# Optimization experiments

Measured on AMD Instinct MI355X. Metric: run time of the kernel, lower is better.

The kernel has to match this reference:

```python
import jax, jax.numpy as jnp
import numpy as np

C = 1.0
TEMPERATURE = 1.0
EPS = 1e-10
N, D = 8192, 512


def setup_inputs() -> dict:
    key = jax.random.key(0)
    k1, k2 = jax.random.split(key)
    # scale so embeddings lie inside the unit (Poincare) ball: norms ~0.5
    scale = 0.5 / np.sqrt(D)
    audio = jax.random.normal(k1, (N, D), dtype=jnp.float32) * scale
    text = jax.random.normal(k2, (N, D), dtype=jnp.float32) * scale
    labels = jnp.arange(N, dtype=jnp.int32)
    return {"audio_features": audio, "text_features": text, "labels": labels}


def _hyperbolic_similarity(a, b):
    # pairwise squared distance via norm expansion (avoids N x N x D tensor)
    a2 = jnp.sum(a * a, axis=-1)            # [N]
    b2 = jnp.sum(b * b, axis=-1)            # [M]
    diff_sq = a2[:, None] + b2[None, :] - 2.0 * (a @ b.T)  # [N, M]
    a2c = jnp.minimum(a2, 1.0 - EPS)
    b2c = jnp.minimum(b2, 1.0 - EPS)
    denom = jnp.maximum((1.0 - a2c)[:, None] * (1.0 - b2c)[None, :], EPS)
    arg = jnp.maximum(1.0 + 2.0 * diff_sq / denom, 1.0 + EPS)
    dist = jnp.arccosh(arg) / jnp.sqrt(jnp.asarray(C, a.dtype))
    return -dist / TEMPERATURE


def _cross_entropy(logits, labels):
    logp = jax.nn.log_softmax(logits, axis=-1)
    picked = jnp.take_along_axis(logp, labels[:, None], axis=-1)[:, 0]
    return -jnp.mean(picked)


def reference(audio_features, text_features, labels):
    sim = _hyperbolic_similarity(audio_features, text_features)  # [N, M]
    loss_audio = _cross_entropy(sim, labels)
    loss_text = _cross_entropy(sim.T, labels)
    return (loss_audio + loss_text) * 0.5
```

## Files before the change

### kernel.cpp

```cpp
#include <hip/hip_runtime.h>
#include <hip/hip_bf16.h>


#define NROWS 8192
#define DDIM  512
#define BM 128
#define BN 128
#define BK 64
#define NT (DDIM / BK)

typedef __attribute__((ext_vector_type(8))) short bf16x8;
typedef __attribute__((ext_vector_type(4))) float f32x4;

constexpr float EPSF = 1e-10f;

#define GLOAD_LDS16(g, l)                                                        \
    __builtin_amdgcn_global_load_lds(                                            \
        (const __attribute__((address_space(1))) void*)(g),                      \
        (__attribute__((address_space(3))) void*)(l), 16, 0, 0)

__device__ inline unsigned short f2bf(float f) {
    union { float f; unsigned int u; } x; x.f = f;
    unsigned int r = x.u + 0x7fffu + ((x.u >> 16) & 1u);
    return (unsigned short)(r >> 16);
}

__global__ __launch_bounds__(256) void convert_norms(const float* __restrict__ audio,
                                                     const float* __restrict__ text,
                                                     unsigned short* __restrict__ Ab,
                                                     unsigned short* __restrict__ Bb,
                                                     float* __restrict__ a2,
                                                     float* __restrict__ b2,
                                                     float* __restrict__ diag) {
    int wave = threadIdx.x >> 6;
    int lane = threadIdx.x & 63;
    int row  = blockIdx.x * 4 + wave;
    const float* ra = audio + (size_t)row * DDIM + lane * 8;
    const float* rt = text  + (size_t)row * DDIM + lane * 8;
    float4 a0 = *(const float4*)(ra), a1 = *(const float4*)(ra + 4);
    float4 t0 = *(const float4*)(rt), t1 = *(const float4*)(rt + 4);

    float sa = a0.x*a0.x + a0.y*a0.y + a0.z*a0.z + a0.w*a0.w
             + a1.x*a1.x + a1.y*a1.y + a1.z*a1.z + a1.w*a1.w;
    float st = t0.x*t0.x + t0.y*t0.y + t0.z*t0.z + t0.w*t0.w
             + t1.x*t1.x + t1.y*t1.y + t1.z*t1.z + t1.w*t1.w;
    float dt = a0.x*t0.x + a0.y*t0.y + a0.z*t0.z + a0.w*t0.w
             + a1.x*t1.x + a1.y*t1.y + a1.z*t1.z + a1.w*t1.w;

    unsigned short ua[8], ut[8];
    ua[0]=f2bf(a0.x); ua[1]=f2bf(a0.y); ua[2]=f2bf(a0.z); ua[3]=f2bf(a0.w);
    ua[4]=f2bf(a1.x); ua[5]=f2bf(a1.y); ua[6]=f2bf(a1.z); ua[7]=f2bf(a1.w);
    ut[0]=f2bf(t0.x); ut[1]=f2bf(t0.y); ut[2]=f2bf(t0.z); ut[3]=f2bf(t0.w);
    ut[4]=f2bf(t1.x); ut[5]=f2bf(t1.y); ut[6]=f2bf(t1.z); ut[7]=f2bf(t1.w);
    *(uint4*)(Ab + (size_t)row * DDIM + lane * 8) = *(const uint4*)ua;
    *(uint4*)(Bb + (size_t)row * DDIM + lane * 8) = *(const uint4*)ut;

    #pragma unroll
    for (int m = 1; m < 64; m <<= 1) {
        sa += __shfl_xor(sa, m);
        st += __shfl_xor(st, m);
        dt += __shfl_xor(dt, m);
    }
    if (lane == 0) {
        a2[row] = sa;
        b2[row] = st;
        float a2c  = fminf(sa, 1.0f - EPSF);
        float b2c  = fminf(st, 1.0f - EPSF);
        float diff = sa + st - 2.0f * dt;
        float den  = fmaxf((1.0f - a2c) * (1.0f - b2c), EPSF);
        float arg  = fmaxf(1.0f + 2.0f * diff / den, 1.0f + EPSF);
        diag[row]  = -logf(arg + sqrtf(arg * arg - 1.0f));
    }
}

__global__ __launch_bounds__(256) void hyper_gemm(
    const unsigned short* __restrict__ A, const unsigned short* __restrict__ B,
    const float* __restrict__ a2, const float* __restrict__ b2,
    float* __restrict__ rowsum, float* __restrict__ colsum) {

    __shared__ char lds[2 * 32768];

    const int tid  = threadIdx.x;
    const int lane = tid & 63;
    const int w    = tid >> 6;
    const int wr   = w >> 1, wc = w & 1;

    const int bid = blockIdx.x;
    const int idx = bid >> 3;
    const int by  = (bid & 7) * 8 + (idx & 7);
    const int bx  = idx >> 3;
    const int i0 = by * BM;
    const int j0 = bx * BN;

    const int g  = lane >> 4;
    const int cl = lane & 15;

    const int srow = lane >> 3;
    const int scol = ((lane & 7) ^ srow) * 8;
    const char* aP[4]; const char* bP[4]; int ldsOff[4];
    #pragma unroll
    for (int c = 0; c < 4; ++c) {
        int row = w * 32 + c * 8 + srow;
        aP[c] = (const char*)(A + (size_t)(i0 + row) * DDIM + scol);
        bP[c] = (const char*)(B + (size_t)(j0 + row) * DDIM + scol);
        ldsOff[c] = w * 4096 + c * 1024;
    }

    int offA[4][2], offB[4][2];
    #pragma unroll
    for (int mi = 0; mi < 4; ++mi) {
        int rowA = wr * 64 + mi * 16 + cl;
        int rowB = wc * 64 + mi * 16 + cl;
        #pragma unroll
        for (int kh = 0; kh < 2; ++kh) {
            int cb = (kh * 32 + g * 8) * 2;
            offA[mi][kh] = rowA * 128 + (cb ^ ((rowA & 7) << 4));
            offB[mi][kh] = 16384 + rowB * 128 + (cb ^ ((rowB & 7) << 4));
        }
    }

    f32x4 acc[4][4];
    #pragma unroll
    for (int mi = 0; mi < 4; ++mi)
        #pragma unroll
        for (int ni = 0; ni < 4; ++ni)
            acc[mi][ni] = (f32x4)0.0f;

#define STAGE(buf, t)                                                     \
    do {                                                                  \
        _Pragma("unroll")                                                 \
        for (int c = 0; c < 4; ++c) {                                     \
            GLOAD_LDS16(aP[c] + (t) * (BK * 2),                           \
                        lds + (buf) * 32768 + ldsOff[c]);                 \
            GLOAD_LDS16(bP[c] + (t) * (BK * 2),                           \
                        lds + (buf) * 32768 + 16384 + ldsOff[c]);         \
        }                                                                 \
    } while (0)

#define COMPUTE(buf)                                                      \
    do {                                                                  \
        _Pragma("unroll")                                                 \
        for (int kh = 0; kh < 2; ++kh) {                                  \
            bf16x8 af[4], bfr[4];                                         \
            _Pragma("unroll")                                             \
            for (int mi = 0; mi < 4; ++mi)                                \
                af[mi] = *(const bf16x8*)(lds + (buf) * 32768 + offA[mi][kh]); \
            _Pragma("unroll")                                             \
            for (int ni = 0; ni < 4; ++ni)                                \
                bfr[ni] = *(const bf16x8*)(lds + (buf) * 32768 + offB[ni][kh]); \
            _Pragma("unroll")                                             \
            for (int mi = 0; mi < 4; ++mi)                                \
                _Pragma("unroll")                                         \
                for (int ni = 0; ni < 4; ++ni)                            \
                    acc[mi][ni] = __builtin_amdgcn_mfma_f32_16x16x32_bf16(\
                        af[mi], bfr[ni], acc[mi][ni], 0, 0, 0);           \
        }                                                                 \
    } while (0)

    STAGE(0, 0);
    __syncthreads();
    #pragma unroll
    for (int t = 0; t < NT; ++t) {
        if (t + 1 < NT) STAGE((t + 1) & 1, t + 1);
        COMPUTE(t & 1);
        if (t + 1 < NT) __syncthreads();
    }
#undef STAGE
#undef COMPUTE

    float B2c[4], fb[4];
    #pragma unroll
    for (int ni = 0; ni < 4; ++ni) {
        float B2 = b2[j0 + wc * 64 + ni * 16 + cl];
        B2c[ni] = B2;
        fb[ni] = __builtin_amdgcn_rcpf(1.0f - fminf(B2, 1.0f - EPSF));
    }

    float cp[4] = {0.f, 0.f, 0.f, 0.f};
    #pragma unroll
    for (int mi = 0; mi < 4; ++mi) {
        #pragma unroll
        for (int reg = 0; reg < 4; ++reg) {
            int   gi  = i0 + wr * 64 + mi * 16 + g * 4 + reg;
            float A2  = a2[gi];
            float fa  = 2.0f * __builtin_amdgcn_rcpf(1.0f - fminf(A2, 1.0f - EPSF));
            float rsum = 0.f;
            #pragma unroll
            for (int ni = 0; ni < 4; ++ni) {
                float dot  = acc[mi][ni][reg];
                float diff = fmaf(-2.0f, dot, A2 + B2c[ni]);
                float arg  = fmaf(diff * fa, fb[ni], 1.0f);
                arg = fmaxf(arg, 1.0f);
                float sq = sqrtf(fmaf(arg, arg, -1.0f));
                float e  = arg - sq;
                rsum += e;
                cp[ni] += e;
            }
            float v = rsum;
            v += __shfl_xor(v, 1); v += __shfl_xor(v, 2);
            v += __shfl_xor(v, 4); v += __shfl_xor(v, 8);
            if (cl == 0) atomicAdd(&rowsum[gi], v);
        }
    }
    #pragma unroll
    for (int ni = 0; ni < 4; ++ni) {
        float v = cp[ni];
        v += __shfl_xor(v, 16); v += __shfl_xor(v, 32);
        if (g == 0) atomicAdd(&colsum[j0 + wc * 64 + ni * 16 + cl], v);
    }
}

__global__ __launch_bounds__(256) void finalize(const float* __restrict__ rowsum,
                                                const float* __restrict__ colsum,
                                                const float* __restrict__ diag,
                                                float* __restrict__ out) {
    int i = blockIdx.x * 256 + threadIdx.x;
    float s = logf(rowsum[i]) + logf(colsum[i]) - 2.0f * diag[i];
    #pragma unroll
    for (int m = 1; m < 64; m <<= 1) s += __shfl_xor(s, m);
    if ((threadIdx.x & 63) == 0)
        atomicAdd(out, s * (1.0f / (2.0f * NROWS)));
}

extern "C" void kernel_launch(void* const* d_in, const int* in_sizes, int n_in,
                              void* d_out, int out_size, void* d_ws, size_t ws_size,
                              hipStream_t stream) {
    const float* audio = (const float*)d_in[0];
    const float* text  = (const float*)d_in[1];
    float* out = (float*)d_out;

    char* ws = (char*)d_ws;
    const size_t BF = (size_t)NROWS * DDIM * sizeof(unsigned short);
    unsigned short* Abf = (unsigned short*)ws;
    unsigned short* Bbf = (unsigned short*)(ws + BF);
    float* a2     = (float*)(ws + 2 * BF);
    float* b2     = a2 + NROWS;
    float* rowsum = b2 + NROWS;
    float* colsum = rowsum + NROWS;
    float* diag   = colsum + NROWS;

    hipMemsetAsync(rowsum, 0, 2 * NROWS * sizeof(float), stream);
    hipMemsetAsync(out, 0, sizeof(float), stream);
    convert_norms<<<NROWS / 4, 256, 0, stream>>>(audio, text, Abf, Bbf, a2, b2, diag);
    hyper_gemm<<<(NROWS / BM) * (NROWS / BN), 256, 0, stream>>>(Abf, Bbf, a2, b2, rowsum, colsum);
    finalize<<<NROWS / 256, 256, 0, stream>>>(rowsum, colsum, diag, out);
}
```

Measured before the change: 227.0 us.

## Enlarge GEMM tile to 256x256 with 8 waves per block

Doubles the block tile to 256x256 with 512 threads (8 waves in a 2x4 layout), each wave computing a 128x64 sub-tile. LDS staging per buffer doubles to 64 KB, and the block-index swizzle is reworked for the 32x32 grid. The goal is more data reuse per LDS byte and fewer atomic partial-sum writes. In exchange, accumulator register use doubles, the 128 KB of LDS allows only one block per CU, and the grid shrinks to 1024 blocks, which may hurt latency hiding.

```diff
diff --git a/kernel.cpp b/kernel.cpp
--- a/kernel.cpp
+++ b/kernel.cpp
@@ -4,10 +4,11 @@
 
 #define NROWS 8192
 #define DDIM  512
-#define BM 128
-#define BN 128
+#define BM 256
+#define BN 256
 #define BK 64
 #define NT (DDIM / BK)
+#define LDSBUF 65536
 
 typedef __attribute__((ext_vector_type(8))) short bf16x8;
 typedef __attribute__((ext_vector_type(4))) float f32x4;
@@ -73,22 +74,23 @@
     }
 }
 
-__global__ __launch_bounds__(256) void hyper_gemm(
+__global__ __launch_bounds__(512) void hyper_gemm(
     const unsigned short* __restrict__ A, const unsigned short* __restrict__ B,
     const float* __restrict__ a2, const float* __restrict__ b2,
     float* __restrict__ rowsum, float* __restrict__ colsum) {
 
-    __shared__ char lds[2 * 32768];
+    __shared__ char lds[2 * LDSBUF];
 
     const int tid  = threadIdx.x;
     const int lane = tid & 63;
     const int w    = tid >> 6;
-    const int wr   = w >> 1, wc = w & 1;
+    const int wm   = w >> 2;
+    const int wn   = w & 3;
 
     const int bid = blockIdx.x;
-    const int idx = bid >> 3;
-    const int by  = (bid & 7) * 8 + (idx & 7);
-    const int bx  = idx >> 3;
+    const int swz = (bid & 7) * 128 + (bid >> 3);
+    const int by  = swz >> 5;
+    const int bx  = swz & 31;
     const int i0 = by * BM;
     const int j0 = bx * BN;
 
@@ -106,22 +108,29 @@
         ldsOff[c] = w * 4096 + c * 1024;
     }
 
-    int offA[4][2], offB[4][2];
-    #pragma unroll
-    for (int mi = 0; mi < 4; ++mi) {
-        int rowA = wr * 64 + mi * 16 + cl;
-        int rowB = wc * 64 + mi * 16 + cl;
+    int offA[8][2], offB[4][2];
+    #pragma unroll
+    for (int mi = 0; mi < 8; ++mi) {
+        int rowA = wm * 128 + mi * 16 + cl;
         #pragma unroll
         for (int kh = 0; kh < 2; ++kh) {
             int cb = (kh * 32 + g * 8) * 2;
             offA[mi][kh] = rowA * 128 + (cb ^ ((rowA & 7) << 4));
-            offB[mi][kh] = 16384 + rowB * 128 + (cb ^ ((rowB & 7) << 4));
         }
     }
-
-    f32x4 acc[4][4];
-    #pragma unroll
-    for (int mi = 0; mi < 4; ++mi)
+    #pragma unroll
+    for (int ni = 0; ni < 4; ++ni) {
+        int rowB = wn * 64 + ni * 16 + cl;
+        #pragma unroll
+        for (int kh = 0; kh < 2; ++kh) {
+            int cb = (kh * 32 + g * 8) * 2;
+            offB[ni][kh] = 32768 + rowB * 128 + (cb ^ ((rowB & 7) << 4));
+        }
+    }
+
+    f32x4 acc[8][4];
+    #pragma unroll
+    for (int mi = 0; mi < 8; ++mi)
         #pragma unroll
         for (int ni = 0; ni < 4; ++ni)
             acc[mi][ni] = (f32x4)0.0f;
@@ -131,9 +140,9 @@
         _Pragma("unroll")                                                 \
         for (int c = 0; c < 4; ++c) {                                     \
             GLOAD_LDS16(aP[c] + (t) * (BK * 2),                           \
-                        lds + (buf) * 32768 + ldsOff[c]);                 \
+                        lds + (buf) * LDSBUF + ldsOff[c]);                \
             GLOAD_LDS16(bP[c] + (t) * (BK * 2),                           \
-                        lds + (buf) * 32768 + 16384 + ldsOff[c]);         \
+                        lds + (buf) * LDSBUF + 32768 + ldsOff[c]);        \
         }                                                                 \
     } while (0)
 
@@ -141,19 +150,19 @@
     do {                                                                  \
         _Pragma("unroll")                                                 \
         for (int kh = 0; kh < 2; ++kh) {                                  \
-            bf16x8 af[4], bfr[4];                                         \
+            bf16x8 af[8], bv[4];                                          \
             _Pragma("unroll")                                             \
-            for (int mi = 0; mi < 4; ++mi)                                \
-                af[mi] = *(const bf16x8*)(lds + (buf) * 32768 + offA[mi][kh]); \
+            for (int mi = 0; mi < 8; ++mi)                                \
+                af[mi] = *(const bf16x8*)(lds + (buf) * LDSBUF + offA[mi][kh]); \
             _Pragma("unroll")                                             \
             for (int ni = 0; ni < 4; ++ni)                                \
-                bfr[ni] = *(const bf16x8*)(lds + (buf) * 32768 + offB[ni][kh]); \
+                bv[ni] = *(const bf16x8*)(lds + (buf) * LDSBUF + offB[ni][kh]); \
             _Pragma("unroll")                                             \
-            for (int mi = 0; mi < 4; ++mi)                                \
+            for (int mi = 0; mi < 8; ++mi)                                \
                 _Pragma("unroll")                                         \
                 for (int ni = 0; ni < 4; ++ni)                            \
                     acc[mi][ni] = __builtin_amdgcn_mfma_f32_16x16x32_bf16(\
-                        af[mi], bfr[ni], acc[mi][ni], 0, 0, 0);           \
+                        af[mi], bv[ni], acc[mi][ni], 0, 0, 0);            \
         }                                                                 \
     } while (0)
 
@@ -171,17 +180,17 @@
     float B2c[4], fb[4];
     #pragma unroll
     for (int ni = 0; ni < 4; ++ni) {
-        float B2 = b2[j0 + wc * 64 + ni * 16 + cl];
+        float B2 = b2[j0 + wn * 64 + ni * 16 + cl];
         B2c[ni] = B2;
         fb[ni] = __builtin_amdgcn_rcpf(1.0f - fminf(B2, 1.0f - EPSF));
     }
 
     float cp[4] = {0.f, 0.f, 0.f, 0.f};
     #pragma unroll
-    for (int mi = 0; mi < 4; ++mi) {
+    for (int mi = 0; mi < 8; ++mi) {
         #pragma unroll
         for (int reg = 0; reg < 4; ++reg) {
-            int   gi  = i0 + wr * 64 + mi * 16 + g * 4 + reg;
+            int   gi  = i0 + wm * 128 + mi * 16 + g * 4 + reg;
             float A2  = a2[gi];
             float fa  = 2.0f * __builtin_amdgcn_rcpf(1.0f - fminf(A2, 1.0f - EPSF));
             float rsum = 0.f;
@@ -206,7 +215,7 @@
     for (int ni = 0; ni < 4; ++ni) {
         float v = cp[ni];
         v += __shfl_xor(v, 16); v += __shfl_xor(v, 32);
-        if (g == 0) atomicAdd(&colsum[j0 + wc * 64 + ni * 16 + cl], v);
+        if (g == 0) atomicAdd(&colsum[j0 + wn * 64 + ni * 16 + cl], v);
     }
 }
 
@@ -242,6 +251,6 @@
     hipMemsetAsync(rowsum, 0, 2 * NROWS * sizeof(float), stream);
     hipMemsetAsync(out, 0, sizeof(float), stream);
     convert_norms<<<NROWS / 4, 256, 0, stream>>>(audio, text, Abf, Bbf, a2, b2, diag);
-    hyper_gemm<<<(NROWS / BM) * (NROWS / BN), 256, 0, stream>>>(Abf, Bbf, a2, b2, rowsum, colsum);
+    hyper_gemm<<<(NROWS / BM) * (NROWS / BN), 512, 0, stream>>>(Abf, Bbf, a2, b2, rowsum, colsum);
     finalize<<<NROWS / 256, 256, 0, stream>>>(rowsum, colsum, diag, out);
 }
```

Result: slower. 277.5 us (+22.2%).

## Use 8 waves per GEMM block and single-block finalize reduction

Applied to the files above, without the earlier changes.

The hyperbolic GEMM block grows from 4 to 8 waves. Each wave now computes a 64x32 sub-tile instead of 64x64, which halves the accumulator registers and global-to-LDS loads per wave and is meant to raise latency hiding and occupancy. The finalize step becomes a single 1024-thread block that reduces through shared memory and writes the output directly, removing the output memset and the atomics. The trade-off is more LDS reads per MFMA (the A fragments are re-read by more waves) and more row and column atomics in the epilogue.

```diff
diff --git a/kernel.cpp b/kernel.cpp
--- a/kernel.cpp
+++ b/kernel.cpp
@@ -8,6 +8,7 @@
 #define BN 128
 #define BK 64
 #define NT (DDIM / BK)
+#define LDSBUF 32768
 
 typedef __attribute__((ext_vector_type(8))) short bf16x8;
 typedef __attribute__((ext_vector_type(4))) float f32x4;
@@ -73,17 +74,18 @@
     }
 }
 
-__global__ __launch_bounds__(256) void hyper_gemm(
+__global__ __launch_bounds__(512, 4) void hyper_gemm(
     const unsigned short* __restrict__ A, const unsigned short* __restrict__ B,
     const float* __restrict__ a2, const float* __restrict__ b2,
     float* __restrict__ rowsum, float* __restrict__ colsum) {
 
-    __shared__ char lds[2 * 32768];
+    __shared__ char lds[2 * LDSBUF];
 
     const int tid  = threadIdx.x;
     const int lane = tid & 63;
     const int w    = tid >> 6;
-    const int wr   = w >> 1, wc = w & 1;
+    const int wm   = w >> 2;
+    const int wn   = w & 3;
 
     const int bid = blockIdx.x;
     const int idx = bid >> 3;
@@ -97,43 +99,50 @@
 
     const int srow = lane >> 3;
     const int scol = ((lane & 7) ^ srow) * 8;
-    const char* aP[4]; const char* bP[4]; int ldsOff[4];
-    #pragma unroll
-    for (int c = 0; c < 4; ++c) {
-        int row = w * 32 + c * 8 + srow;
+    const char* aP[2]; const char* bP[2]; int ldsOff[2];
+    #pragma unroll
+    for (int c = 0; c < 2; ++c) {
+        int row = w * 16 + c * 8 + srow;
         aP[c] = (const char*)(A + (size_t)(i0 + row) * DDIM + scol);
         bP[c] = (const char*)(B + (size_t)(j0 + row) * DDIM + scol);
-        ldsOff[c] = w * 4096 + c * 1024;
-    }
-
-    int offA[4][2], offB[4][2];
+        ldsOff[c] = w * 2048 + c * 1024;
+    }
+
+    int offA[4][2], offB[2][2];
     #pragma unroll
     for (int mi = 0; mi < 4; ++mi) {
-        int rowA = wr * 64 + mi * 16 + cl;
-        int rowB = wc * 64 + mi * 16 + cl;
+        int rowA = wm * 64 + mi * 16 + cl;
         #pragma unroll
         for (int kh = 0; kh < 2; ++kh) {
             int cb = (kh * 32 + g * 8) * 2;
             offA[mi][kh] = rowA * 128 + (cb ^ ((rowA & 7) << 4));
-            offB[mi][kh] = 16384 + rowB * 128 + (cb ^ ((rowB & 7) << 4));
         }
     }
-
-    f32x4 acc[4][4];
+    #pragma unroll
+    for (int ni = 0; ni < 2; ++ni) {
+        int rowB = wn * 32 + ni * 16 + cl;
+        #pragma unroll
+        for (int kh = 0; kh < 2; ++kh) {
+            int cb = (kh * 32 + g * 8) * 2;
+            offB[ni][kh] = 16384 + rowB * 128 + (cb ^ ((rowB & 7) << 4));
+        }
+    }
+
+    f32x4 acc[4][2];
     #pragma unroll
     for (int mi = 0; mi < 4; ++mi)
         #pragma unroll
-        for (int ni = 0; ni < 4; ++ni)
+        for (int ni = 0; ni < 2; ++ni)
             acc[mi][ni] = (f32x4)0.0f;
 
 #define STAGE(buf, t)                                                     \
     do {                                                                  \
         _Pragma("unroll")                                                 \
-        for (int c = 0; c < 4; ++c) {                                     \
+        for (int c = 0; c < 2; ++c) {                                     \
             GLOAD_LDS16(aP[c] + (t) * (BK * 2),                           \
-                        lds + (buf) * 32768 + ldsOff[c]);                 \
+                        lds + (buf) * LDSBUF + ldsOff[c]);                \
             GLOAD_LDS16(bP[c] + (t) * (BK * 2),                           \
-                        lds + (buf) * 32768 + 16384 + ldsOff[c]);         \
+                        lds + (buf) * LDSBUF + 16384 + ldsOff[c]);        \
         }                                                                 \
     } while (0)
 
@@ -141,19 +150,19 @@
     do {                                                                  \
         _Pragma("unroll")                                                 \
         for (int kh = 0; kh < 2; ++kh) {                                  \
-            bf16x8 af[4], bfr[4];                                         \
+            bf16x8 af[4], bv[2];                                          \
             _Pragma("unroll")                                             \
             for (int mi = 0; mi < 4; ++mi)                                \
-                af[mi] = *(const bf16x8*)(lds + (buf) * 32768 + offA[mi][kh]); \
+                af[mi] = *(const bf16x8*)(lds + (buf) * LDSBUF + offA[mi][kh]); \
             _Pragma("unroll")                                             \
-            for (int ni = 0; ni < 4; ++ni)                                \
-                bfr[ni] = *(const bf16x8*)(lds + (buf) * 32768 + offB[ni][kh]); \
+            for (int ni = 0; ni < 2; ++ni)                                \
+                bv[ni] = *(const bf16x8*)(lds + (buf) * LDSBUF + offB[ni][kh]); \
             _Pragma("unroll")                                             \
             for (int mi = 0; mi < 4; ++mi)                                \
                 _Pragma("unroll")                                         \
-                for (int ni = 0; ni < 4; ++ni)                            \
+                for (int ni = 0; ni < 2; ++ni)                            \
                     acc[mi][ni] = __builtin_amdgcn_mfma_f32_16x16x32_bf16(\
-                        af[mi], bfr[ni], acc[mi][ni], 0, 0, 0);           \
+                        af[mi], bv[ni], acc[mi][ni], 0, 0, 0);            \
         }                                                                 \
     } while (0)
 
@@ -168,25 +177,25 @@
 #undef STAGE
 #undef COMPUTE
 
-    float B2c[4], fb[4];
-    #pragma unroll
-    for (int ni = 0; ni < 4; ++ni) {
-        float B2 = b2[j0 + wc * 64 + ni * 16 + cl];
+    float B2c[2], fb[2];
+    #pragma unroll
+    for (int ni = 0; ni < 2; ++ni) {
+        float B2 = b2[j0 + wn * 32 + ni * 16 + cl];
         B2c[ni] = B2;
         fb[ni] = __builtin_amdgcn_rcpf(1.0f - fminf(B2, 1.0f - EPSF));
     }
 
-    float cp[4] = {0.f, 0.f, 0.f, 0.f};
+    float cp[2] = {0.f, 0.f};
     #pragma unroll
     for (int mi = 0; mi < 4; ++mi) {
         #pragma unroll
         for (int reg = 0; reg < 4; ++reg) {
-            int   gi  = i0 + wr * 64 + mi * 16 + g * 4 + reg;
+            int   gi  = i0 + wm * 64 + mi * 16 + g * 4 + reg;
             float A2  = a2[gi];
             float fa  = 2.0f * __builtin_amdgcn_rcpf(1.0f - fminf(A2, 1.0f - EPSF));
             float rsum = 0.f;
             #pragma unroll
-            for (int ni = 0; ni < 4; ++ni) {
+            for (int ni = 0; ni < 2; ++ni) {
                 float dot  = acc[mi][ni][reg];
                 float diff = fmaf(-2.0f, dot, A2 + B2c[ni]);
                 float arg  = fmaf(diff * fa, fb[ni], 1.0f);
@@ -203,23 +212,32 @@
         }
     }
     #pragma unroll
-    for (int ni = 0; ni < 4; ++ni) {
+    for (int ni = 0; ni < 2; ++ni) {
         float v = cp[ni];
         v += __shfl_xor(v, 16); v += __shfl_xor(v, 32);
-        if (g == 0) atomicAdd(&colsum[j0 + wc * 64 + ni * 16 + cl], v);
-    }
-}
-
-__global__ __launch_bounds__(256) void finalize(const float* __restrict__ rowsum,
-                                                const float* __restrict__ colsum,
-                                                const float* __restrict__ diag,
-                                                float* __restrict__ out) {
-    int i = blockIdx.x * 256 + threadIdx.x;
-    float s = logf(rowsum[i]) + logf(colsum[i]) - 2.0f * diag[i];
+        if (g == 0) atomicAdd(&colsum[j0 + wn * 32 + ni * 16 + cl], v);
+    }
+}
+
+__global__ __launch_bounds__(1024) void finalize(const float* __restrict__ rowsum,
+                                                 const float* __restrict__ colsum,
+                                                 const float* __restrict__ diag,
+                                                 float* __restrict__ out) {
+    float s = 0.f;
+    for (int i = threadIdx.x; i < NROWS; i += 1024)
+        s += logf(rowsum[i]) + logf(colsum[i]) - 2.0f * diag[i];
+    __shared__ float red[16];
+    int lane = threadIdx.x & 63, wv = threadIdx.x >> 6;
     #pragma unroll
     for (int m = 1; m < 64; m <<= 1) s += __shfl_xor(s, m);
-    if ((threadIdx.x & 63) == 0)
-        atomicAdd(out, s * (1.0f / (2.0f * NROWS)));
+    if (lane == 0) red[wv] = s;
+    __syncthreads();
+    if (threadIdx.x == 0) {
+        float t = 0.f;
+        #pragma unroll
+        for (int k = 0; k < 16; ++k) t += red[k];
+        out[0] = t / (2.0f * NROWS);
+    }
 }
 
 extern "C" void kernel_launch(void* const* d_in, const int* in_sizes, int n_in,
@@ -240,8 +258,7 @@
     float* diag   = colsum + NROWS;
 
     hipMemsetAsync(rowsum, 0, 2 * NROWS * sizeof(float), stream);
-    hipMemsetAsync(out, 0, sizeof(float), stream);
     convert_norms<<<NROWS / 4, 256, 0, stream>>>(audio, text, Abf, Bbf, a2, b2, diag);
-    hyper_gemm<<<(NROWS / BM) * (NROWS / BN), 256, 0, stream>>>(Abf, Bbf, a2, b2, rowsum, colsum);
-    finalize<<<NROWS / 256, 256, 0, stream>>>(rowsum, colsum, diag, out);
-}
+    hyper_gemm<<<(NROWS / BM) * (NROWS / BN), 512, 0, stream>>>(Abf, Bbf, a2, b2, rowsum, colsum);
+    finalize<<<1, 1024, 0, stream>>>(rowsum, colsum, diag, out);
+}
```

Result: no change. 229.1 us (+0.9%).
